# Performance work log

Hardware: AMD Instinct MI355X
Metric: run time of the kernel (lower is better)

The kernel has to match this reference:

```python
import jax, jax.numpy as jnp
import numpy as np

TOP_K = 8


def setup_inputs() -> dict:
    key = jax.random.key(0)
    k1, k2 = jax.random.split(key)
    hidden_states = jax.random.normal(k1, (16384, 2048), dtype=jnp.float32)
    weight = jax.random.normal(k2, (64, 2048), dtype=jnp.float32) * 0.02
    return {"hidden_states": hidden_states, "weight": weight}


def reference(hidden_states, weight):
    # router_logits = F.linear(hidden_states, weight): [T, E]
    router_logits = jnp.einsum('th,eh->te', hidden_states, weight)
    # softmax in float32 as in the original
    router_probs = jax.nn.softmax(router_logits.astype(jnp.float32), axis=-1)
    router_top_values, router_indices = jax.lax.top_k(router_probs, TOP_K)
    # norm_topk_prob=True: renormalize selected probs to sum to 1
    router_top_values = router_top_values / jnp.sum(router_top_values, axis=-1, keepdims=True)
    return (router_logits,
            router_top_values.astype(hidden_states.dtype),
            router_indices)
```

## Files before the change

### kernel.cpp

```cpp
#include <hip/hip_runtime.h>
#include <math.h>

#define T_TOKENS 16384
#define HID      2048
#define NE       64
#define TOPK     8
#define TM       32
#define BK       128
#define NCH      (HID / BK)
#define RSTR     272
#define A_SPL    8704
#define B_SPL    17408
#define B_OFF    26112
#define LDS_BYTES 78336

typedef float  f32x4  __attribute__((ext_vector_type(4)));
typedef short  short8 __attribute__((ext_vector_type(8)));

#define MFMA16(A, B, C) __builtin_amdgcn_mfma_f32_16x16x32_bf16((A), (B), (C), 0, 0, 0)

static __device__ __forceinline__ unsigned short f2bf(float x) {
    unsigned u = __builtin_bit_cast(unsigned, x);
    return (unsigned short)((u + 0x7FFFu + ((u >> 16) & 1u)) >> 16);
}
static __device__ __forceinline__ float bf2f(unsigned short h) {
    unsigned u = ((unsigned)h) << 16;
    return __builtin_bit_cast(float, u);
}
static __device__ __forceinline__ void split1(float x, unsigned short& h0,
                                              unsigned short& h1, unsigned short& h2) {
    h0 = f2bf(x); float r = x - bf2f(h0);
    h1 = f2bf(r); r = r - bf2f(h1);
    h2 = f2bf(r);
}
#define SPLIT4(V, B, S0, S1, S2) do {                                             \
    unsigned short h0_, h1_, h2_;                                                 \
    split1((V).x, h0_, h1_, h2_); (S0)[(B)+0]=(short)h0_; (S1)[(B)+0]=(short)h1_; (S2)[(B)+0]=(short)h2_; \
    split1((V).y, h0_, h1_, h2_); (S0)[(B)+1]=(short)h0_; (S1)[(B)+1]=(short)h1_; (S2)[(B)+1]=(short)h2_; \
    split1((V).z, h0_, h1_, h2_); (S0)[(B)+2]=(short)h0_; (S1)[(B)+2]=(short)h1_; (S2)[(B)+2]=(short)h2_; \
    split1((V).w, h0_, h1_, h2_); (S0)[(B)+3]=(short)h0_; (S1)[(B)+3]=(short)h1_; (S2)[(B)+3]=(short)h2_; \
} while (0)

__global__ __launch_bounds__(256, 2) void router_kernel(
    const float* __restrict__ hidden,
    const float* __restrict__ weight,
    float* __restrict__ out_logits,
    float* __restrict__ out_vals,
    float* __restrict__ out_idxf)
{
    __shared__ __align__(16) char smem[LDS_BYTES];
    double (*lg)[NE + 1] = reinterpret_cast<double(*)[NE + 1]>(smem);

    const int tid  = threadIdx.x;
    const int tok0 = blockIdx.x * TM;
    const int lane = tid & 63;
    const int wave = tid >> 6;
    const int tw   = wave & 1;
    const int eh   = wave >> 1;

    const int fr = lane & 15;
    const int fk = lane >> 4;

    int rowmap[4], colmap[4];
    {
        const unsigned short mb = f2bf((float)fr);
        const unsigned short ob = f2bf(0.03125f);
        short8 vm, vo;
        #pragma unroll
        for (int j = 0; j < 8; ++j) { vm[j] = (short)mb; vo[j] = (short)ob; }
        const f32x4 z = {0.f, 0.f, 0.f, 0.f};
        const f32x4 pr = MFMA16(vm, vo, z);
        const f32x4 pc = MFMA16(vo, vm, z);
        #pragma unroll
        for (int i = 0; i < 4; ++i) {
            rowmap[i] = (int)(pr[i] + 0.5f);
            colmap[i] = (int)(pc[i] + 0.5f);
        }
    }

    const int ar    = tid >> 3;
    const int ac16  = (tid & 7) * 16;
    const int be    = tid >> 2;
    const int bslot = tid & 3;

    const float* aG = hidden + (size_t)(tok0 + ar) * HID + ac16;
    const float* bG = weight + (size_t)be * HID + bslot * 32;
    char* const  aW = smem + ar * RSTR + 2 * ac16;
    char* const  bW = smem + B_OFF + be * RSTR + (bslot << 6);

    const int aBase = (tw * 16 + fr) * RSTR + fk * 16;
    const int bBase = B_OFF + (eh * 32 + fr) * RSTR + fk * 16;

    const f32x4 z4 = {0.f, 0.f, 0.f, 0.f};
    f32x4 acch0 = z4, acch1 = z4;
    f32x4 accl0 = z4, accl1 = z4;
    double accd0[4] = {0, 0, 0, 0}, accd1[4] = {0, 0, 0, 0};

    float4 pa[4], pb[8];

#define STAGE() do {                                                              \
    short8 sa0a, sa0b, sa1a, sa1b, sa2a, sa2b;                                    \
    SPLIT4(pa[0], 0, sa0a, sa1a, sa2a); SPLIT4(pa[1], 4, sa0a, sa1a, sa2a);       \
    SPLIT4(pa[2], 0, sa0b, sa1b, sa2b); SPLIT4(pa[3], 4, sa0b, sa1b, sa2b);       \
    *(short8*)(aW            ) = sa0a;  *(short8*)(aW             + 16) = sa0b;   \
    *(short8*)(aW +   A_SPL  ) = sa1a;  *(short8*)(aW +   A_SPL   + 16) = sa1b;   \
    *(short8*)(aW + 2*A_SPL  ) = sa2a;  *(short8*)(aW + 2*A_SPL   + 16) = sa2b;   \
    short8 sb0[4], sb1[4], sb2[4];                                                \
    SPLIT4(pb[0], 0, sb0[0], sb1[0], sb2[0]); SPLIT4(pb[1], 4, sb0[0], sb1[0], sb2[0]); \
    SPLIT4(pb[2], 0, sb0[1], sb1[1], sb2[1]); SPLIT4(pb[3], 4, sb0[1], sb1[1], sb2[1]); \
    SPLIT4(pb[4], 0, sb0[2], sb1[2], sb2[2]); SPLIT4(pb[5], 4, sb0[2], sb1[2], sb2[2]); \
    SPLIT4(pb[6], 0, sb0[3], sb1[3], sb2[3]); SPLIT4(pb[7], 4, sb0[3], sb1[3], sb2[3]); \
    _Pragma("unroll")                                                             \
    for (int q_ = 0; q_ < 4; ++q_) {                                              \
        *(short8*)(bW             + 16 * q_) = sb0[q_];                           \
        *(short8*)(bW +   B_SPL   + 16 * q_) = sb1[q_];                           \
        *(short8*)(bW + 2*B_SPL   + 16 * q_) = sb2[q_];                           \
    }                                                                             \
} while (0)

    #pragma unroll
    for (int q = 0; q < 4; ++q) pa[q] = *(const float4*)(aG + 4 * q);
    #pragma unroll
    for (int q = 0; q < 8; ++q) pb[q] = *(const float4*)(bG + 4 * q);
    STAGE();
    __syncthreads();

    for (int c = 0; c < NCH; ++c) {
        if (c + 1 < NCH) {
            const int off = (c + 1) * BK;
            #pragma unroll
            for (int q = 0; q < 4; ++q) pa[q] = *(const float4*)(aG + off + 4 * q);
            #pragma unroll
            for (int q = 0; q < 8; ++q) pb[q] = *(const float4*)(bG + off + 4 * q);
        }

        #pragma unroll
        for (int st = 0; st < 4; ++st) {
            const int ao = aBase + st * 64;
            const short8 A0 = *(const short8*)(smem + ao);
            const short8 A1 = *(const short8*)(smem + A_SPL + ao);
            const short8 A2 = *(const short8*)(smem + 2 * A_SPL + ao);
            const int bo = bBase + st * 64;
            const short8 B00 = *(const short8*)(smem + bo);
            const short8 B01 = *(const short8*)(smem + bo + 16 * RSTR);
            const short8 B10 = *(const short8*)(smem + B_SPL + bo);
            const short8 B11 = *(const short8*)(smem + B_SPL + bo + 16 * RSTR);
            const short8 B20 = *(const short8*)(smem + 2 * B_SPL + bo);
            const short8 B21 = *(const short8*)(smem + 2 * B_SPL + bo + 16 * RSTR);
            acch0 = MFMA16(A0, B00, acch0);  acch1 = MFMA16(A0, B01, acch1);
            accl0 = MFMA16(A0, B10, accl0);  accl1 = MFMA16(A0, B11, accl1);
            accl0 = MFMA16(A1, B00, accl0);  accl1 = MFMA16(A1, B01, accl1);
            accl0 = MFMA16(A1, B10, accl0);  accl1 = MFMA16(A1, B11, accl1);
            accl0 = MFMA16(A0, B20, accl0);  accl1 = MFMA16(A0, B21, accl1);
            accl0 = MFMA16(A2, B00, accl0);  accl1 = MFMA16(A2, B01, accl1);
        }

        #pragma unroll
        for (int i = 0; i < 4; ++i) {
            accd0[i] += (double)acch0[i];
            accd1[i] += (double)acch1[i];
        }
        acch0 = z4; acch1 = z4;

        __syncthreads();
        if (c + 1 < NCH) STAGE();
        __syncthreads();
    }

    #pragma unroll
    for (int i = 0; i < 4; ++i) {
        const int trow = tw * 16 + rowmap[i];
        const int tok  = tok0 + trow;
        const int e0   = eh * 32 + colmap[i];
        const double l0 = accd0[i] + (double)accl0[i];
        const double l1 = accd1[i] + (double)accl1[i];
        out_logits[(size_t)tok * NE + e0]      = (float)l0;
        out_logits[(size_t)tok * NE + e0 + 16] = (float)l1;
        lg[trow][e0]      = l0;
        lg[trow][e0 + 16] = l1;
    }
    __syncthreads();

    for (int tt = wave; tt < TM; tt += 4) {
        double cur = lg[tt][lane];
        double first = 0.0;
        float  s = 0.f, myv = 0.f;
        int myi = 0;
        #pragma unroll
        for (int i = 0; i < TOPK; ++i) {
            double mv = cur;
            #pragma unroll
            for (int off = 32; off; off >>= 1) {
                const double ov = __shfl_xor(mv, off);
                mv = ov > mv ? ov : mv;
            }
            const unsigned long long m = __ballot(cur == mv);
            const int mi = __ffsll(m) - 1;
            if (i == 0) first = mv;
            const float e = expf((float)(mv - first));
            s += e;
            if (lane == i)  { myv = e; myi = mi; }
            if (lane == mi) cur = -INFINITY;
        }
        if (lane < TOPK) {
            const int tok = tok0 + tt;
            out_vals[(size_t)tok * TOPK + lane] = myv / s;
            out_idxf[(size_t)tok * TOPK + lane] = (float)myi;
        }
    }
}

extern "C" void kernel_launch(void* const* d_in, const int* in_sizes, int n_in,
                              void* d_out, int out_size, void* d_ws, size_t ws_size,
                              hipStream_t stream) {
    const float* hidden = (const float*)d_in[0];
    const float* weight = (const float*)d_in[1];

    float* out        = (float*)d_out;
    float* out_logits = out;
    float* out_vals   = out + (size_t)T_TOKENS * NE;
    float* out_idxf   = out + (size_t)T_TOKENS * NE + (size_t)T_TOKENS * TOPK;

    dim3 grid(T_TOKENS / TM);
    dim3 block(256);
    hipLaunchKernelGGL(router_kernel, grid, block, 0, stream,
                       hidden, weight, out_logits, out_vals, out_idxf);
}
```

Before: 235.3 us.

## Pre-split weight into MFMA fragment layout and read B from global; double-buffer A

```diff
diff --git a/kernel.cpp b/kernel.cpp
--- a/kernel.cpp
+++ b/kernel.cpp
@@ -9,10 +9,11 @@
 #define BK       128
 #define NCH      (HID / BK)
 #define RSTR     272
-#define A_SPL    8704
-#define B_SPL    17408
-#define B_OFF    26112
-#define LDS_BYTES 78336
+#define A_SPL    (32 * RSTR)
+#define ABUF     (3 * A_SPL)
+#define LDS_BYTES (2 * ABUF)
+
+#define WS_SHORT8 49152
 
 typedef float  f32x4  __attribute__((ext_vector_type(4)));
 typedef short  short8 __attribute__((ext_vector_type(8)));
@@ -41,9 +42,28 @@
     split1((V).w, h0_, h1_, h2_); (S0)[(B)+3]=(short)h0_; (S1)[(B)+3]=(short)h1_; (S2)[(B)+3]=(short)h2_; \
 } while (0)
 
+__global__ __launch_bounds__(256) void split_weight_kernel(
+    const float* __restrict__ weight, short8* __restrict__ ws8)
+{
+    const int n = blockIdx.x;
+    const int o = threadIdx.x;
+    const float4 w0 = *(const float4*)&weight[(size_t)n * HID + o * 8];
+    const float4 w1 = *(const float4*)&weight[(size_t)n * HID + o * 8 + 4];
+    short8 s0, s1, s2;
+    SPLIT4(w0, 0, s0, s1, s2);
+    SPLIT4(w1, 4, s0, s1, s2);
+    const int t    = o >> 2;
+    const int lane = (o & 3) * 16 + (n & 15);
+    const int e    = n >> 4;
+    const int base = t * 256 + e * 64 + lane;
+    ws8[base]         = s0;
+    ws8[base + 16384] = s1;
+    ws8[base + 32768] = s2;
+}
+
 __global__ __launch_bounds__(256, 2) void router_kernel(
     const float* __restrict__ hidden,
-    const float* __restrict__ weight,
+    const short8* __restrict__ bfrag,
     float* __restrict__ out_logits,
     float* __restrict__ out_vals,
     float* __restrict__ out_idxf)
@@ -78,75 +98,58 @@
         }
     }
 
-    const int ar    = tid >> 3;
-    const int ac16  = (tid & 7) * 16;
-    const int be    = tid >> 2;
-    const int bslot = tid & 3;
-
+    const int ar   = tid >> 3;
+    const int ac16 = (tid & 7) * 16;
     const float* aG = hidden + (size_t)(tok0 + ar) * HID + ac16;
-    const float* bG = weight + (size_t)be * HID + bslot * 32;
-    char* const  aW = smem + ar * RSTR + 2 * ac16;
-    char* const  bW = smem + B_OFF + be * RSTR + (bslot << 6);
-
-    const int aBase = (tw * 16 + fr) * RSTR + fk * 16;
-    const int bBase = B_OFF + (eh * 32 + fr) * RSTR + fk * 16;
+    const int aWOff = ar * RSTR + ac16 * 2;
+
+    const short8* bP = bfrag + eh * 128 + lane;
+
+    const int aOff = (tw * 16 + fr) * RSTR + fk * 16;
 
     const f32x4 z4 = {0.f, 0.f, 0.f, 0.f};
     f32x4 acch0 = z4, acch1 = z4;
     f32x4 accl0 = z4, accl1 = z4;
     double accd0[4] = {0, 0, 0, 0}, accd1[4] = {0, 0, 0, 0};
 
-    float4 pa[4], pb[8];
-
-#define STAGE() do {                                                              \
-    short8 sa0a, sa0b, sa1a, sa1b, sa2a, sa2b;                                    \
-    SPLIT4(pa[0], 0, sa0a, sa1a, sa2a); SPLIT4(pa[1], 4, sa0a, sa1a, sa2a);       \
-    SPLIT4(pa[2], 0, sa0b, sa1b, sa2b); SPLIT4(pa[3], 4, sa0b, sa1b, sa2b);       \
-    *(short8*)(aW            ) = sa0a;  *(short8*)(aW             + 16) = sa0b;   \
-    *(short8*)(aW +   A_SPL  ) = sa1a;  *(short8*)(aW +   A_SPL   + 16) = sa1b;   \
-    *(short8*)(aW + 2*A_SPL  ) = sa2a;  *(short8*)(aW + 2*A_SPL   + 16) = sa2b;   \
-    short8 sb0[4], sb1[4], sb2[4];                                                \
-    SPLIT4(pb[0], 0, sb0[0], sb1[0], sb2[0]); SPLIT4(pb[1], 4, sb0[0], sb1[0], sb2[0]); \
-    SPLIT4(pb[2], 0, sb0[1], sb1[1], sb2[1]); SPLIT4(pb[3], 4, sb0[1], sb1[1], sb2[1]); \
-    SPLIT4(pb[4], 0, sb0[2], sb1[2], sb2[2]); SPLIT4(pb[5], 4, sb0[2], sb1[2], sb2[2]); \
-    SPLIT4(pb[6], 0, sb0[3], sb1[3], sb2[3]); SPLIT4(pb[7], 4, sb0[3], sb1[3], sb2[3]); \
-    _Pragma("unroll")                                                             \
-    for (int q_ = 0; q_ < 4; ++q_) {                                              \
-        *(short8*)(bW             + 16 * q_) = sb0[q_];                           \
-        *(short8*)(bW +   B_SPL   + 16 * q_) = sb1[q_];                           \
-        *(short8*)(bW + 2*B_SPL   + 16 * q_) = sb2[q_];                           \
-    }                                                                             \
-} while (0)
-
-    #pragma unroll
-    for (int q = 0; q < 4; ++q) pa[q] = *(const float4*)(aG + 4 * q);
-    #pragma unroll
-    for (int q = 0; q < 8; ++q) pb[q] = *(const float4*)(bG + 4 * q);
-    STAGE();
+    float4 pa[4];
+
+    {
+        #pragma unroll
+        for (int q = 0; q < 4; ++q) pa[q] = *(const float4*)(aG + 4 * q);
+        short8 sa0a, sa0b, sa1a, sa1b, sa2a, sa2b;
+        SPLIT4(pa[0], 0, sa0a, sa1a, sa2a); SPLIT4(pa[1], 4, sa0a, sa1a, sa2a);
+        SPLIT4(pa[2], 0, sa0b, sa1b, sa2b); SPLIT4(pa[3], 4, sa0b, sa1b, sa2b);
+        char* aW = smem + aWOff;
+        *(short8*)(aW            ) = sa0a;  *(short8*)(aW             + 16) = sa0b;
+        *(short8*)(aW +   A_SPL  ) = sa1a;  *(short8*)(aW +   A_SPL   + 16) = sa1b;
+        *(short8*)(aW + 2*A_SPL  ) = sa2a;  *(short8*)(aW + 2*A_SPL   + 16) = sa2b;
+    }
     __syncthreads();
 
     for (int c = 0; c < NCH; ++c) {
+        const int cur = c & 1;
+        const char* bufc = smem + cur * ABUF;
+
         if (c + 1 < NCH) {
             const int off = (c + 1) * BK;
             #pragma unroll
             for (int q = 0; q < 4; ++q) pa[q] = *(const float4*)(aG + off + 4 * q);
-            #pragma unroll
-            for (int q = 0; q < 8; ++q) pb[q] = *(const float4*)(bG + off + 4 * q);
         }
 
         #pragma unroll
         for (int st = 0; st < 4; ++st) {
-            const int ao = aBase + st * 64;
-            const short8 A0 = *(const short8*)(smem + ao);
-            const short8 A1 = *(const short8*)(smem + A_SPL + ao);
-            const short8 A2 = *(const short8*)(smem + 2 * A_SPL + ao);
-            const int bo = bBase + st * 64;
-            const short8 B00 = *(const short8*)(smem + bo);
-            const short8 B01 = *(const short8*)(smem + bo + 16 * RSTR);
-            const short8 B10 = *(const short8*)(smem + B_SPL + bo);
-            const short8 B11 = *(const short8*)(smem + B_SPL + bo + 16 * RSTR);
-            const short8 B20 = *(const short8*)(smem + 2 * B_SPL + bo);
-            const short8 B21 = *(const short8*)(smem + 2 * B_SPL + bo + 16 * RSTR);
+            const int t  = c * 4 + st;
+            const int ao = aOff + st * 64;
+            const short8 A0 = *(const short8*)(bufc + ao);
+            const short8 A1 = *(const short8*)(bufc + A_SPL + ao);
+            const short8 A2 = *(const short8*)(bufc + 2 * A_SPL + ao);
+            const short8 B00 = bP[t * 256];
+            const short8 B01 = bP[t * 256 + 64];
+            const short8 B10 = bP[t * 256 + 16384];
+            const short8 B11 = bP[t * 256 + 16384 + 64];
+            const short8 B20 = bP[t * 256 + 32768];
+            const short8 B21 = bP[t * 256 + 32768 + 64];
             acch0 = MFMA16(A0, B00, acch0);  acch1 = MFMA16(A0, B01, acch1);
             accl0 = MFMA16(A0, B10, accl0);  accl1 = MFMA16(A0, B11, accl1);
             accl0 = MFMA16(A1, B00, accl0);  accl1 = MFMA16(A1, B01, accl1);
@@ -162,8 +165,15 @@
         }
         acch0 = z4; acch1 = z4;
 
-        __syncthreads();
-        if (c + 1 < NCH) STAGE();
+        if (c + 1 < NCH) {
+            short8 sa0a, sa0b, sa1a, sa1b, sa2a, sa2b;
+            SPLIT4(pa[0], 0, sa0a, sa1a, sa2a); SPLIT4(pa[1], 4, sa0a, sa1a, sa2a);
+            SPLIT4(pa[2], 0, sa0b, sa1b, sa2b); SPLIT4(pa[3], 4, sa0b, sa1b, sa2b);
+            char* aW = smem + (cur ^ 1) * ABUF + aWOff;
+            *(short8*)(aW            ) = sa0a;  *(short8*)(aW             + 16) = sa0b;
+            *(short8*)(aW +   A_SPL  ) = sa1a;  *(short8*)(aW +   A_SPL   + 16) = sa1b;
+            *(short8*)(aW + 2*A_SPL  ) = sa2a;  *(short8*)(aW + 2*A_SPL   + 16) = sa2b;
+        }
         __syncthreads();
     }
 
@@ -221,8 +231,10 @@
     float* out_vals   = out + (size_t)T_TOKENS * NE;
     float* out_idxf   = out + (size_t)T_TOKENS * NE + (size_t)T_TOKENS * TOPK;
 
-    dim3 grid(T_TOKENS / TM);
-    dim3 block(256);
-    hipLaunchKernelGGL(router_kernel, grid, block, 0, stream,
-                       hidden, weight, out_logits, out_vals, out_idxf);
-}
+    short8* ws8 = (short8*)d_ws;
+
+    hipLaunchKernelGGL(split_weight_kernel, dim3(NE), dim3(256), 0, stream,
+                       weight, ws8);
+    hipLaunchKernelGGL(router_kernel, dim3(T_TOKENS / TM), dim3(256), 0, stream,
+                       hidden, (const short8*)ws8, out_logits, out_vals, out_idxf);
+}
```

Result: no change. 233.2 us (-0.9%).
